# Kernel tuning notes

Hardware: AMD Instinct MI355X
Metric: run time of the kernel (lower is better)

The kernel has to match this reference:

```python
import jax, jax.numpy as jnp
import numpy as np

N_QUBITS = 7  # fixed in source


def setup_inputs() -> dict:
    key = jax.random.key(0)
    ks = jax.random.split(key, 9)
    B, F = 131072, 64
    return {
        "x_q": jax.random.normal(ks[0], (B, N_QUBITS), jnp.float32),
        "x_c": jax.random.normal(ks[1], (B, F), jnp.float32),
        "q_params": jax.random.normal(ks[2], (N_QUBITS,), jnp.float32),
        "W1": jax.random.normal(ks[3], (1 + F, 32), jnp.float32) * 0.1,
        "b1": jnp.zeros((32,), jnp.float32),
        "W2": jax.random.normal(ks[4], (32, 16), jnp.float32) * 0.1,
        "b2": jnp.zeros((16,), jnp.float32),
        "W3": jax.random.normal(ks[5], (16, 1), jnp.float32) * 0.1,
        "b3": jnp.zeros((1,), jnp.float32),
    }


def _cnot(state, c, t):
    # state: [B, 2,2,2,2,2,2,2]; wire q lives on axis q+1 (wire 0 most significant,
    # matching pennylane default.qubit ordering). CNOT flips target where control=1.
    s = jnp.moveaxis(state, (1 + c, 1 + t), (1, 2))
    s = jnp.stack([s[:, 0], s[:, 1, ::-1]], axis=1)
    return jnp.moveaxis(s, (1, 2), (1 + c, 1 + t))


def _quantum_expval_z0(x_q, q_params):
    B = x_q.shape[0]
    # RY(x)RY(w) on same wire == RY(x+w); RY(theta)|0> = cos(t/2)|0> + sin(t/2)|1>
    half = (x_q + q_params[None, :]) * 0.5
    amp = jnp.stack([jnp.cos(half), jnp.sin(half)], axis=-1)  # [B, 7, 2], real state
    state = amp[:, 0]  # [B, 2]
    for q in range(1, N_QUBITS):  # batched product state via outer products
        state = (state[:, :, None] * amp[:, q, None, :]).reshape(B, -1)
    state = state.reshape((B,) + (2,) * N_QUBITS)
    for i in range(N_QUBITS):  # ring of CNOTs: (0,1),(1,2),...,(6,0)
        state = _cnot(state, i, (i + 1) % N_QUBITS)
    p = state.reshape(B, 2, -1) ** 2  # probabilities split on wire 0
    return p[:, 0].sum(-1) - p[:, 1].sum(-1)  # <Z_0>, shape [B]


def reference(x_q, x_c, q_params, W1, b1, W2, b2, W3, b3):
    q_out = _quantum_expval_z0(x_q, q_params)  # [B]
    combined = jnp.concatenate([q_out[:, None], x_c], axis=1)  # [B, 1+F]
    h = jax.nn.relu(combined @ W1 + b1)
    h = jax.nn.relu(h @ W2 + b2)
    return (h @ W3 + b3)[:, 0]  # squeeze(-1)
```

## Files before the change

### kernel.cpp

```cpp
#include <hip/hip_runtime.h>
#include <hip/hip_bf16.h>


#define NQ 7
#define F  64
#define H1 32
#define H2 16

#define L1_BODY(XV, WPTR)                                                    \
    do {                                                                     \
        const float* w_ = (WPTR);                                            \
        _Pragma("unroll")                                                    \
        for (int j = 0; j < H1; ++j) acc1[j] = fmaf((XV).x, w_[j],          acc1[j]); \
        _Pragma("unroll")                                                    \
        for (int j = 0; j < H1; ++j) acc1[j] = fmaf((XV).y, w_[H1 + j],     acc1[j]); \
        _Pragma("unroll")                                                    \
        for (int j = 0; j < H1; ++j) acc1[j] = fmaf((XV).z, w_[2 * H1 + j], acc1[j]); \
        _Pragma("unroll")                                                    \
        for (int j = 0; j < H1; ++j) acc1[j] = fmaf((XV).w, w_[3 * H1 + j], acc1[j]); \
    } while (0)

__global__ __launch_bounds__(256) void hybrid_fused(
    const float* __restrict__ x_q, const float* __restrict__ x_c,
    const float* __restrict__ q_params,
    const float* __restrict__ W1, const float* __restrict__ b1,
    const float* __restrict__ W2, const float* __restrict__ b2,
    const float* __restrict__ W3, const float* __restrict__ b3,
    float* __restrict__ out, int B)
{
    const int row = blockIdx.x * 256 + threadIdx.x;
    if (row >= B) return;

    float qv = 1.0f;
    #pragma unroll
    for (int q = 1; q < NQ; ++q) {
        qv *= __cosf(x_q[(size_t)row * NQ + q] + q_params[q]);
    }

    float acc1[H1];
    #pragma unroll
    for (int j = 0; j < H1; ++j)
        acc1[j] = fmaf(qv, W1[j], b1[j]);

    const float4* xc4 = reinterpret_cast<const float4*>(x_c + (size_t)row * F);

    float4 cur = xc4[0];
    #pragma unroll 1
    for (int k4 = 0; k4 < F / 4 - 1; ++k4) {
        const float4 nxt = xc4[k4 + 1];
        L1_BODY(cur, W1 + (size_t)(1 + 4 * k4) * H1);
        cur = nxt;
    }
    L1_BODY(cur, W1 + (size_t)(1 + 4 * (F / 4 - 1)) * H1);

    float acc2[H2];
    #pragma unroll
    for (int j = 0; j < H2; ++j) acc2[j] = b2[j];
    #pragma unroll
    for (int k = 0; k < H1; ++k) {
        const float h = fmaxf(acc1[k], 0.0f);
        #pragma unroll
        for (int j = 0; j < H2; ++j)
            acc2[j] = fmaf(h, W2[k * H2 + j], acc2[j]);
    }

    float o = b3[0];
    #pragma unroll
    for (int k = 0; k < H2; ++k)
        o = fmaf(fmaxf(acc2[k], 0.0f), W3[k], o);

    out[row] = o;
}

extern "C" void kernel_launch(void* const* d_in, const int* in_sizes, int n_in,
                              void* d_out, int out_size, void* d_ws, size_t ws_size,
                              hipStream_t stream) {
    const float* x_q      = (const float*)d_in[0];
    const float* x_c      = (const float*)d_in[1];
    const float* q_params = (const float*)d_in[2];
    const float* W1       = (const float*)d_in[3];
    const float* b1       = (const float*)d_in[4];
    const float* W2       = (const float*)d_in[5];
    const float* b2       = (const float*)d_in[6];
    const float* W3       = (const float*)d_in[7];
    const float* b3       = (const float*)d_in[8];
    float* out = (float*)d_out;

    const int B = in_sizes[0] / NQ;
    const int grid = (B + 255) / 256;

    hybrid_fused<<<grid, 256, 0, stream>>>(x_q, x_c, q_params,
                                           W1, b1, W2, b2, W3, b3,
                                           out, B);
}
```

Measured before the change: 105.1 us.

## Split layer-1 reduction across two waves per row with LDS combine

Each row is now handled by two wavefronts, each accumulating half of the 64 input features for the first dense layer. One half writes its partial sums to shared memory, and after a barrier the other half adds them and finishes layers 2 and 3. This doubles the thread count and halves the serial FMA chain per thread to expose more parallelism. In exchange it adds shared-memory traffic, a block-wide sync, and idle waves during the tail computation.

New measurement: 125.6 us. 1.2x slower.

```diff
diff --git a/kernel.cpp b/kernel.cpp
--- a/kernel.cpp
+++ b/kernel.cpp
@@ -6,6 +6,7 @@
 #define F  64
 #define H1 32
 #define H2 16
+#define RPB 128
 
 #define L1_BODY(XV, WPTR)                                                    \
     do {                                                                     \
@@ -28,30 +29,57 @@
     const float* __restrict__ W3, const float* __restrict__ b3,
     float* __restrict__ out, int B)
 {
-    const int row = blockIdx.x * 256 + threadIdx.x;
-    if (row >= B) return;
+    __shared__ float part[RPB][H1 + 1];
 
-    float qv = 1.0f;
-    #pragma unroll
-    for (int q = 1; q < NQ; ++q) {
-        qv *= __cosf(x_q[(size_t)row * NQ + q] + q_params[q]);
+    const int tid  = threadIdx.x;
+    const int wid  = tid >> 6;
+    const int lane = tid & 63;
+    const int half = wid & 1;
+    const int lrow = (wid >> 1) * 64 + lane;
+    const int row  = blockIdx.x * RPB + lrow;
+    const bool active = (row < B);
+
+    float acc1[H1];
+
+    if (active) {
+        if (half == 0) {
+            float qv = 1.0f;
+            #pragma unroll
+            for (int q = 1; q < NQ; ++q)
+                qv *= __cosf(x_q[(size_t)row * NQ + q] + q_params[q]);
+            #pragma unroll
+            for (int j = 0; j < H1; ++j)
+                acc1[j] = fmaf(qv, W1[j], b1[j]);
+        } else {
+            #pragma unroll
+            for (int j = 0; j < H1; ++j) acc1[j] = 0.0f;
+        }
+
+        const float4* xc4 = reinterpret_cast<const float4*>(
+            x_c + (size_t)row * F + half * (F / 2));
+        const float* wbase = W1 + (size_t)(1 + half * (F / 2)) * H1;
+
+        float4 cur = xc4[0];
+        #pragma unroll 1
+        for (int k4 = 0; k4 < F / 8 - 1; ++k4) {
+            const float4 nxt = xc4[k4 + 1];
+            L1_BODY(cur, wbase + (size_t)(4 * k4) * H1);
+            cur = nxt;
+        }
+        L1_BODY(cur, wbase + (size_t)(4 * (F / 8 - 1)) * H1);
+
+        if (half == 1) {
+            #pragma unroll
+            for (int j = 0; j < H1; ++j) part[lrow][j] = acc1[j];
+        }
     }
 
-    float acc1[H1];
+    __syncthreads();
+
+    if (half == 1 || !active) return;
+
     #pragma unroll
-    for (int j = 0; j < H1; ++j)
-        acc1[j] = fmaf(qv, W1[j], b1[j]);
-
-    const float4* xc4 = reinterpret_cast<const float4*>(x_c + (size_t)row * F);
-
-    float4 cur = xc4[0];
-    #pragma unroll 1
-    for (int k4 = 0; k4 < F / 4 - 1; ++k4) {
-        const float4 nxt = xc4[k4 + 1];
-        L1_BODY(cur, W1 + (size_t)(1 + 4 * k4) * H1);
-        cur = nxt;
-    }
-    L1_BODY(cur, W1 + (size_t)(1 + 4 * (F / 4 - 1)) * H1);
+    for (int j = 0; j < H1; ++j) acc1[j] += part[lrow][j];
 
     float acc2[H2];
     #pragma unroll
@@ -87,7 +115,7 @@
     float* out = (float*)d_out;
 
     const int B = in_sizes[0] / NQ;
-    const int grid = (B + 255) / 256;
+    const int grid = (B + RPB - 1) / RPB;
 
     hybrid_fused<<<grid, 256, 0, stream>>>(x_q, x_c, q_params,
                                            W1, b1, W2, b2, W3, b3,
```

## Stage x_c rows into LDS via async global_load_lds with XOR swizzle

Applied to the files above, without the earlier changes.

Replaces per-thread strided float4 loads of each row's x_c with coalesced asynchronous global-to-LDS copies (global_load_lds, 16 bytes each), where each wave fetches its 64 rows into a 16KB per-wave shared tile using an XOR swizzle to avoid bank conflicts. The first half of the features is consumed after a partial vmcnt wait so compute overlaps the second half's load. This removes uncoalesced per-lane row-strided global accesses, at the cost of 64KB of LDS per block, which limits occupancy. It also drops the row>=B bounds check, so it assumes B is a multiple of 256.

Result: no change. 105.2 us (+0.1%).

```diff
diff --git a/kernel.cpp b/kernel.cpp
--- a/kernel.cpp
+++ b/kernel.cpp
@@ -1,11 +1,15 @@
 #include <hip/hip_runtime.h>
-#include <hip/hip_bf16.h>
 
 
 #define NQ 7
 #define F  64
 #define H1 32
 #define H2 16
+
+#define GLL16(GSRC, LDST)                                                    \
+    __builtin_amdgcn_global_load_lds(                                        \
+        (const __attribute__((address_space(1))) void*)(GSRC),               \
+        (__attribute__((address_space(3))) void*)(LDST), 16, 0, 0)
 
 #define L1_BODY(XV, WPTR)                                                    \
     do {                                                                     \
@@ -28,30 +32,52 @@
     const float* __restrict__ W3, const float* __restrict__ b3,
     float* __restrict__ out, int B)
 {
-    const int row = blockIdx.x * 256 + threadIdx.x;
-    if (row >= B) return;
+    __shared__ __align__(16) float tile[4 * 4096];
+
+    const int tid  = threadIdx.x;
+    const int lane = tid & 63;
+    const int w    = tid >> 6;
+    const size_t blk_row0 = (size_t)blockIdx.x * 256;
+    const size_t row = blk_row0 + tid;
 
     float qv = 1.0f;
     #pragma unroll
-    for (int q = 1; q < NQ; ++q) {
-        qv *= __cosf(x_q[(size_t)row * NQ + q] + q_params[q]);
-    }
+    for (int q = 1; q < NQ; ++q)
+        qv *= __cosf(x_q[row * NQ + q] + q_params[q]);
 
     float acc1[H1];
     #pragma unroll
     for (int j = 0; j < H1; ++j)
         acc1[j] = fmaf(qv, W1[j], b1[j]);
 
-    const float4* xc4 = reinterpret_cast<const float4*>(x_c + (size_t)row * F);
+    const int s_hi = lane >> 3;
+    const int s_lo = lane & 7;
+    const int cqx  = s_lo ^ s_hi;
+    const float* gbase = x_c + (blk_row0 + (size_t)w * 64 + s_hi) * F + cqx * 4;
+    float* lbase = tile + w * 4096;
 
-    float4 cur = xc4[0];
+    #pragma unroll
+    for (int h = 0; h < 2; ++h)
+        #pragma unroll
+        for (int c = 0; c < 8; ++c)
+            GLL16(gbase + (size_t)c * 8 * F + h * 32,
+                  lbase + h * 2048 + c * 256);
+
+    asm volatile("s_waitcnt vmcnt(8)" ::: "memory");
+    const float4* lrow = reinterpret_cast<const float4*>(lbase)
+                         + s_hi * 64 + s_lo * 8;
     #pragma unroll 1
-    for (int k4 = 0; k4 < F / 4 - 1; ++k4) {
-        const float4 nxt = xc4[k4 + 1];
-        L1_BODY(cur, W1 + (size_t)(1 + 4 * k4) * H1);
-        cur = nxt;
+    for (int k4 = 0; k4 < 8; ++k4) {
+        const float4 xv = lrow[k4 ^ s_lo];
+        L1_BODY(xv, W1 + (size_t)(1 + 4 * k4) * H1);
     }
-    L1_BODY(cur, W1 + (size_t)(1 + 4 * (F / 4 - 1)) * H1);
+
+    asm volatile("s_waitcnt vmcnt(0)" ::: "memory");
+    #pragma unroll 1
+    for (int k4 = 0; k4 < 8; ++k4) {
+        const float4 xv = lrow[512 + (k4 ^ s_lo)];
+        L1_BODY(xv, W1 + (size_t)(1 + 32 + 4 * k4) * H1);
+    }
 
     float acc2[H2];
     #pragma unroll
```
